# Kernel optimization log

Hardware: AMD Instinct MI355X
Metric: run time of the kernel (lower is better)

## Reference

```python
import jax, jax.numpy as jnp
import numpy as np

B, S, C = 256, 169, 512      # batch, input seq_len (hardcoded 169 in source), n_attn
H, TT, HS = 256, 256, 16     # n_head, ctx_len, head_size (all forced by hardcoded shapes)
OUT = 64                     # output Linear(16, 64)


def setup_inputs() -> dict:
    key = jax.random.key(0)
    ks = jax.random.split(key, 13)
    s_in = 1.0 / np.sqrt(C)
    s_hs = 1.0 / np.sqrt(HS)
    return {
        "x": jax.random.normal(ks[0], (B, S, C), dtype=jnp.float32),
        "time_w": jax.random.normal(ks[1], (H, TT), dtype=jnp.float32) * 0.1,
        "time_alpha": jax.random.normal(ks[2], (H, 1, TT), dtype=jnp.float32) * 0.1 + 1.0,
        "time_beta": jax.random.normal(ks[3], (H, TT, 1), dtype=jnp.float32) * 0.1 + 1.0,
        "time_gamma": jax.random.normal(ks[4], (TT, 1), dtype=jnp.float32) * 0.1 + 1.0,
        "key_w": jax.random.normal(ks[5], (HS, C), dtype=jnp.float32) * s_in,
        "key_b": jax.random.normal(ks[6], (HS,), dtype=jnp.float32) * s_in,
        "value_w": jax.random.normal(ks[7], (HS, C), dtype=jnp.float32) * s_in,
        "value_b": jax.random.normal(ks[8], (HS,), dtype=jnp.float32) * s_in,
        "recep_w": jax.random.normal(ks[9], (HS, C), dtype=jnp.float32) * s_in,
        "recep_b": jax.random.normal(ks[10], (HS,), dtype=jnp.float32) * s_in,
        "out_w": jax.random.normal(ks[11], (OUT, HS), dtype=jnp.float32) * s_hs,
        "out_b": jax.random.normal(ks[12], (OUT,), dtype=jnp.float32) * s_hs,
    }


def reference(x, time_w, time_alpha, time_beta, time_gamma,
              key_w, key_b, value_w, value_b, recep_w, recep_b,
              out_w, out_b):
    # --- build the time-decay matrix via the pad/tile shift trick ---
    w = jnp.pad(time_w, ((0, 0), (0, TT)))            # (H, 2TT)
    w = jnp.tile(w, (1, TT))                          # (H, 2TT*TT)
    w = w[:, :-TT].reshape(H, TT, 2 * TT - 1)
    w = w[:, :, TT - 1:]                              # (H, TT, TT)
    w = w * time_alpha * time_beta                    # (H, TT, TT)

    # --- channel-half time shift: first C/2 channels shifted back by 1 step ---
    half = C // 2
    shifted = jnp.pad(x[:, :, :half], ((0, 0), (1, 0), (0, 0)))[:, :-1]
    x = jnp.concatenate([shifted, x[:, :, half:]], axis=-1)

    # --- projections (torch Linear: y = x @ W.T + b) ---
    k = x @ key_w.T + key_b                           # (B, S, HS)
    v = x @ value_w.T + value_b
    r = x @ recep_w.T + recep_b

    pad_len = TT - S                                  # 256 - 169 = 87
    r = jnp.pad(r, ((0, 0), (0, pad_len), (0, 0)))    # (B, TT, HS)

    k = jnp.exp(jnp.clip(k, -60.0, 30.0))
    sum_k = jnp.cumsum(k, axis=1)                     # (B, S, HS)
    sum_k = jnp.pad(sum_k, ((0, 0), (0, pad_len), (0, 0)))  # (B, TT, HS)

    kv = k * v                                        # (B, S, HS)
    kv = jnp.pad(kv, ((0, 0), (0, pad_len), (0, 0)))  # (B, TT, HS)

    # einsum('htu,bhc->btc') == contract u first, then (t,h) matmul against kv's seq axis
    w2 = w.sum(axis=-1)                               # (H, TT): sum_u w[h,t,u]
    wkv = jnp.einsum('ht,bhc->btc', w2, kv)           # (B, TT, HS)

    # original divides by zero-padded sum_k in the padded tail; guard with 1 there
    denom = jnp.where(sum_k == 0, jnp.ones_like(sum_k), sum_k)
    rwkv = jax.nn.sigmoid(r) * wkv / denom            # (B, TT, HS)

    rwkv = rwkv @ out_w.T + out_b                     # (B, TT, 64)
    rwkv = rwkv * time_gamma[:TT]                     # (TT,1) broadcast
    return rwkv
```

## Files before the change

kernel.cpp:

```cpp
#include <hip/hip_runtime.h>

typedef unsigned short u16;
typedef unsigned int u32;
typedef __attribute__((ext_vector_type(8))) __bf16 bf16x8;
typedef __attribute__((ext_vector_type(4))) float f32x4;

#define S_LEN 169
#define C_DIM 512
#define SP 192

#define WT_OFF  0
#define XT0_OFF 49152
#define XT1_OFF 71680
#define KE_OFF  0
#define KVF_OFF 11264
#define RF_OFF  22528
#define KVT_OFF 33792
#define G_OFF   39936
#define RB_OFF  51200
#define SS_OFF  71680
#define OW_OFF  72704
#define LDS_BYTES 94208

#define LGKM_BAR() asm volatile("s_waitcnt lgkmcnt(0)\n\ts_barrier" ::: "memory")

__global__ __launch_bounds__(1024) void w2_kernel(
    const float* __restrict__ time_w,
    const float* __restrict__ time_alpha,
    const float* __restrict__ time_beta,
    __bf16* __restrict__ w2t)
{
    __shared__ float tw[256];
    __shared__ float al[256];
    __shared__ float part[4][256];
    const int s = blockIdx.x;
    const int t = threadIdx.x & 255;
    const int p = threadIdx.x >> 8;
    if (s >= S_LEN) {
        if (p == 0) w2t[t * SP + s] = (__bf16)0.f;
        return;
    }
    if (p == 0) { tw[t] = time_w[s * 256 + t]; al[t] = time_alpha[s * 256 + t]; }
    __syncthreads();
    const int u0 = p << 6;
    const int u1 = (u0 + 64 < t + 1) ? (u0 + 64) : (t + 1);
    float acc = 0.f;
    for (int u = u0; u < u1; ++u)
        acc = fmaf(tw[255 + u - t], al[u], acc);
    part[p][t] = acc;
    __syncthreads();
    if (p == 0)
        w2t[t * SP + s] = (__bf16)(time_beta[s * 256 + t] *
                                   (part[0][t] + part[1][t] + part[2][t] + part[3][t]));
}

__global__ __launch_bounds__(512) void rwkv_main(
    const float* __restrict__ x,
    const float* __restrict__ key_w, const float* __restrict__ key_b,
    const float* __restrict__ value_w, const float* __restrict__ value_b,
    const float* __restrict__ recep_w, const float* __restrict__ recep_b,
    const float* __restrict__ out_w, const float* __restrict__ out_b,
    const float* __restrict__ gamma,
    const __bf16* __restrict__ w2t,
    float* __restrict__ out)
{
    __shared__ __align__(16) char smem[LDS_BYTES];
    const int tid  = threadIdx.x;
    const int lane = tid & 63;
    const int wid  = tid >> 6;
    const int q    = lane >> 4;
    const int hs   = lane & 15;
    const int b    = blockIdx.x;
    const float* xb = x + (size_t)b * (S_LEN * C_DIM);

    for (int i = tid; i < 3072; i += 512) {
        int j  = i >> 6;
        int co = (i & 63) << 3;
        const float* src;
        if (j < 16)      src = key_w   + j * 512 + co;
        else if (j < 32) src = value_w + (j - 16) * 512 + co;
        else             src = recep_w + (j - 32) * 512 + co;
        float4 f0 = *(const float4*)src;
        float4 f1 = *(const float4*)(src + 4);
        bf16x8 p;
        p[0]=(__bf16)f0.x; p[1]=(__bf16)f0.y; p[2]=(__bf16)f0.z; p[3]=(__bf16)f0.w;
        p[4]=(__bf16)f1.x; p[5]=(__bf16)f1.y; p[6]=(__bf16)f1.z; p[7]=(__bf16)f1.w;
        u32 off = (((u32)j << 10) + ((u32)co << 1)) ^ (((u32)(j & 7)) << 4);
        *(bf16x8*)(smem + WT_OFF + off) = p;
    }

    const float kb = key_b[hs];
    const float vb = value_b[hs];
    const float rb = recep_b[hs];

    f32x4 acc0[3], acc1[3];
    #pragma unroll
    for (int n = 0; n < 3; ++n) { acc0[n] = (f32x4){0.f,0.f,0.f,0.f}; acc1[n] = (f32x4){0.f,0.f,0.f,0.f}; }
    const bool has_m1 = (wid < 3);

    float4 pfA[3][2]; int pvA[3];
    float4 pfB[3][2]; int pvB[3];

    auto ldchunk = [&](int chunk, float4 (&pf)[3][2], int (&pv)[3]) {
        const bool shifted = chunk < 4;
        #pragma unroll
        for (int it = 0; it < 3; ++it) {
            int i = tid + (it << 9);
            pv[it] = 0;
            if (i < 1408) {
                int r = i >> 3;
                int tsrc = shifted ? (r - 1) : r;
                bool valid = shifted ? (r >= 1 && r <= S_LEN) : (r < S_LEN);
                pv[it] = 1;
                if (valid) {
                    const float* src = xb + (size_t)tsrc * C_DIM + (chunk << 6) + ((i & 7) << 3);
                    pf[it][0] = *(const float4*)src;
                    pf[it][1] = *(const float4*)(src + 4);
                    pv[it] = 2;
                }
            }
        }
    };

    auto cvtwrite = [&](u32 base, float4 (&pf)[3][2], int (&pv)[3]) {
        #pragma unroll
        for (int it = 0; it < 3; ++it) {
            int i = tid + (it << 9);
            if (i < 1408 && pv[it]) {
                int r = i >> 3, co = (i & 7) << 3;
                bf16x8 p = {(__bf16)0.f,(__bf16)0.f,(__bf16)0.f,(__bf16)0.f,
                            (__bf16)0.f,(__bf16)0.f,(__bf16)0.f,(__bf16)0.f};
                if (pv[it] == 2) {
                    p[0]=(__bf16)pf[it][0].x; p[1]=(__bf16)pf[it][0].y;
                    p[2]=(__bf16)pf[it][0].z; p[3]=(__bf16)pf[it][0].w;
                    p[4]=(__bf16)pf[it][1].x; p[5]=(__bf16)pf[it][1].y;
                    p[6]=(__bf16)pf[it][1].z; p[7]=(__bf16)pf[it][1].w;
                }
                u32 off = (((u32)r << 7) + ((u32)co << 1)) ^ (((u32)(r & 7)) << 4);
                *(bf16x8*)(smem + base + off) = p;
            }
        }
    };

    auto mfma_chunk = [&](int chunk, u32 xbase) {
        #pragma unroll
        for (int ks = 0; ks < 2; ++ks) {
            int kc = ks << 5;
            bf16x8 bfr[3];
            #pragma unroll
            for (int nt = 0; nt < 3; ++nt) {
                int j = nt * 16 + hs;
                u32 col = (u32)((chunk << 6) + kc + (q << 3));
                u32 off = (((u32)j << 10) + (col << 1)) ^ (((u32)(j & 7)) << 4);
                bfr[nt] = *(const bf16x8*)(smem + WT_OFF + off);
            }
            {
                int row = wid * 16 + hs;
                u32 off = (((u32)row << 7) + ((u32)(kc + (q << 3)) << 1)) ^ (((u32)(row & 7)) << 4);
                bf16x8 afr = *(const bf16x8*)(smem + xbase + off);
                acc0[0] = __builtin_amdgcn_mfma_f32_16x16x32_bf16(afr, bfr[0], acc0[0], 0,0,0);
                acc0[1] = __builtin_amdgcn_mfma_f32_16x16x32_bf16(afr, bfr[1], acc0[1], 0,0,0);
                acc0[2] = __builtin_amdgcn_mfma_f32_16x16x32_bf16(afr, bfr[2], acc0[2], 0,0,0);
            }
            if (has_m1) {
                int row = (wid + 8) * 16 + hs;
                u32 off = (((u32)row << 7) + ((u32)(kc + (q << 3)) << 1)) ^ (((u32)(row & 7)) << 4);
                bf16x8 afr = *(const bf16x8*)(smem + xbase + off);
                acc1[0] = __builtin_amdgcn_mfma_f32_16x16x32_bf16(afr, bfr[0], acc1[0], 0,0,0);
                acc1[1] = __builtin_amdgcn_mfma_f32_16x16x32_bf16(afr, bfr[1], acc1[1], 0,0,0);
                acc1[2] = __builtin_amdgcn_mfma_f32_16x16x32_bf16(afr, bfr[2], acc1[2], 0,0,0);
            }
        }
    };

    ldchunk(0, pfA, pvA);
    cvtwrite(XT0_OFF, pfA, pvA);
    ldchunk(1, pfA, pvA);
    ldchunk(2, pfB, pvB);
    LGKM_BAR();

    #pragma unroll
    for (int chunk = 0; chunk < 8; ++chunk) {
        const u32 cur = (chunk & 1) ? XT1_OFF : XT0_OFF;
        const u32 nxt = (chunk & 1) ? XT0_OFF : XT1_OFF;
        mfma_chunk(chunk, cur);
        if (chunk < 7) {
            if (chunk & 1) cvtwrite(nxt, pfB, pvB);
            else           cvtwrite(nxt, pfA, pvA);
        }
        LGKM_BAR();
        if (chunk < 5) {
            if (chunk & 1) ldchunk(chunk + 3, pfB, pvB);
            else           ldchunk(chunk + 3, pfA, pvA);
        }
    }

    float* kef = (float*)(smem + KE_OFF);
    float* kvf = (float*)(smem + KVF_OFF);
    float* rff = (float*)(smem + RF_OFF);
    #pragma unroll
    for (int m = 0; m < 2; ++m) {
        if (m == 1 && !has_m1) break;
        const f32x4* A = (m == 0) ? acc0 : acc1;
        int tb = (wid + m * 8) * 16 + (q << 2);
        float ke[4];
        #pragma unroll
        for (int rg = 0; rg < 4; ++rg) {
            float kk = A[0][rg] + kb;
            kk = fminf(fmaxf(kk, -60.f), 30.f);
            ke[rg] = __expf(kk);
        }
        #pragma unroll
        for (int rg = 0; rg < 4; ++rg) {
            int t = tb + rg;
            kef[t * 16 + hs] = ke[rg];
            kvf[t * 16 + hs] = ke[rg] * (A[1][rg] + vb);
            rff[t * 16 + hs] = A[2][rg] + rb;
        }
    }
    __syncthreads();

    float* seg = (float*)(smem + SS_OFF);
    float* g   = (float*)(smem + G_OFF);
    if (tid < 256) {
        int h = tid & 15, sg = tid >> 4;
        int t0 = sg * 11, t1 = (t0 + 11 < S_LEN) ? t0 + 11 : S_LEN;
        float s = 0.f;
        for (int t = t0; t < t1; ++t) s += kef[t * 16 + h];
        seg[sg * 16 + h] = s;
    } else {
        int i2 = tid - 256;
        for (int i = i2; i < 4096; i += 256) {
            int row = i >> 4, c = 16 + (i & 15);
            ((__bf16*)(smem + RB_OFF))[row * 40 + c] = (__bf16)0.f;
        }
        for (int i = i2; i < 368; i += 256) {
            int h2 = i & 15; int t = S_LEN + (i >> 4);
            u32 off = ((u32)(h2 * 384 + t * 2)) ^ (((u32)(h2 & 7)) << 4);
            *(__bf16*)(smem + KVT_OFF + off) = (__bf16)0.f;
        }
        for (int i = i2; i < 2560; i += 256) {
            int o = i / 40, c = i - o * 40;
            ((__bf16*)(smem + OW_OFF))[o * 40 + c] = (c < 16) ? (__bf16)out_w[o * 16 + c] : (__bf16)0.f;
        }
    }
    __syncthreads();

    if (tid < 256) {
        int h = tid & 15, sg = tid >> 4;
        float run = 0.f;
        for (int s2 = 0; s2 < sg; ++s2) run += seg[s2 * 16 + h];
        int t0 = sg * 11, t1 = (t0 + 11 < S_LEN) ? t0 + 11 : S_LEN;
        for (int t = t0; t < t1; ++t) {
            run += kef[t * 16 + h];
            u32 off = ((u32)(h * 384 + t * 2)) ^ (((u32)(h & 7)) << 4);
            *(__bf16*)(smem + KVT_OFF + off) = (__bf16)kvf[t * 16 + h];
            float rr = rff[t * 16 + h];
            g[t * 16 + h] = 1.f / ((1.f + __expf(-rr)) * run);
        }
    }
    __syncthreads();

    f32x4 wa0 = (f32x4){0.f,0.f,0.f,0.f};
    f32x4 wa1 = (f32x4){0.f,0.f,0.f,0.f};
    #pragma unroll
    for (int s0 = 0; s0 < SP; s0 += 32) {
        int scol = s0 + (q << 3);
        u32 boff = ((u32)(hs * 384 + scol * 2)) ^ (((u32)(hs & 7)) << 4);
        bf16x8 bfr = *(const bf16x8*)(smem + KVT_OFF + boff);
        {
            int row = wid * 16 + hs;
            bf16x8 afr = *(const bf16x8*)(w2t + row * SP + scol);
            wa0 = __builtin_amdgcn_mfma_f32_16x16x32_bf16(afr, bfr, wa0, 0,0,0);
        }
        {
            int row = (wid + 8) * 16 + hs;
            bf16x8 afr = *(const bf16x8*)(w2t + row * SP + scol);
            wa1 = __builtin_amdgcn_mfma_f32_16x16x32_bf16(afr, bfr, wa1, 0,0,0);
        }
    }
    #pragma unroll
    for (int m = 0; m < 2; ++m) {
        const f32x4& W = (m == 0) ? wa0 : wa1;
        int tb = (wid + m * 8) * 16 + (q << 2);
        #pragma unroll
        for (int rg = 0; rg < 4; ++rg) {
            int t = tb + rg;
            float fac = (t < S_LEN) ? g[t * 16 + hs] : 0.5f;
            ((__bf16*)(smem + RB_OFF))[t * 40 + hs] = (__bf16)(W[rg] * fac);
        }
    }
    __syncthreads();

    float obv[4];
    #pragma unroll
    for (int nt = 0; nt < 4; ++nt) obv[nt] = out_b[nt * 16 + hs];
    #pragma unroll
    for (int m = 0; m < 2; ++m) {
        int mt = wid + m * 8;
        int arow = mt * 16 + hs;
        bf16x8 afr = *(const bf16x8*)(smem + RB_OFF + (u32)(arow * 80 + (q << 4)));
        float gm[4];
        #pragma unroll
        for (int rg = 0; rg < 4; ++rg) gm[rg] = gamma[mt * 16 + (q << 2) + rg];
        #pragma unroll
        for (int nt = 0; nt < 4; ++nt) {
            int orow = nt * 16 + hs;
            bf16x8 bfr = *(const bf16x8*)(smem + OW_OFF + (u32)(orow * 80 + (q << 4)));
            f32x4 zc = (f32x4){0.f,0.f,0.f,0.f};
            f32x4 d = __builtin_amdgcn_mfma_f32_16x16x32_bf16(afr, bfr, zc, 0,0,0);
            #pragma unroll
            for (int rg = 0; rg < 4; ++rg) {
                int t = mt * 16 + (q << 2) + rg;
                out[(size_t)b * 16384 + (size_t)t * 64 + nt * 16 + hs] = (d[rg] + obv[nt]) * gm[rg];
            }
        }
    }
}

extern "C" void kernel_launch(void* const* d_in, const int* in_sizes, int n_in,
                              void* d_out, int out_size, void* d_ws, size_t ws_size,
                              hipStream_t stream) {
    const float* x          = (const float*)d_in[0];
    const float* time_w     = (const float*)d_in[1];
    const float* time_alpha = (const float*)d_in[2];
    const float* time_beta  = (const float*)d_in[3];
    const float* time_gamma = (const float*)d_in[4];
    const float* key_w      = (const float*)d_in[5];
    const float* key_b      = (const float*)d_in[6];
    const float* value_w    = (const float*)d_in[7];
    const float* value_b    = (const float*)d_in[8];
    const float* recep_w    = (const float*)d_in[9];
    const float* recep_b    = (const float*)d_in[10];
    const float* out_w      = (const float*)d_in[11];
    const float* out_b      = (const float*)d_in[12];
    __bf16* w2t = (__bf16*)d_ws;

    w2_kernel<<<192, 1024, 0, stream>>>(time_w, time_alpha, time_beta, w2t);
    rwkv_main<<<256, 512, 0, stream>>>(x, key_w, key_b, value_w, value_b,
                                       recep_w, recep_b, out_w, out_b,
                                       time_gamma, w2t, (float*)d_out);
}
```

Before: 38.06 us.

## Split fused RWKV kernel into projection GEMM and scan kernels with workspace handoff

The single per-batch kernel is split into a GEMM kernel that handles half a sequence per block (512 blocks of 256 threads) and a separate scan/output kernel. The QKV weight bf16 packing moves into extra blocks of the w2 precompute kernel, so GEMM blocks copy pre-packed weights instead of converting them. The sigmoid is computed in the GEMM epilogue. The aim is more parallelism and less per-block LDS for the projection stage, at the cost of a global round-trip for k, kv and sigmoid(r) and an extra kernel launch.

```diff
diff --git a/kernel.cpp b/kernel.cpp
--- a/kernel.cpp
+++ b/kernel.cpp
@@ -6,21 +6,27 @@
 typedef __attribute__((ext_vector_type(4))) float f32x4;
 
 #define S_LEN 169
-#define C_DIM 512
 #define SP 192
+
+#define W2T_WS 0
+#define WPK_WS 98304
+#define KE_WS  147456
+#define KV_WS  3031040
+#define SG_WS  5914624
 
 #define WT_OFF  0
 #define XT0_OFF 49152
-#define XT1_OFF 71680
-#define KE_OFF  0
-#define KVF_OFF 11264
-#define RF_OFF  22528
-#define KVT_OFF 33792
-#define G_OFF   39936
-#define RB_OFF  51200
-#define SS_OFF  71680
-#define OW_OFF  72704
-#define LDS_BYTES 94208
+#define XT1_OFF 61440
+#define G_LDS   73728
+
+#define SKE  0
+#define SKV  11264
+#define SG2  22528
+#define SKVT 33792
+#define SRB  39936
+#define SSS  60416
+#define SOW  61440
+#define S_LDS 66560
 
 #define LGKM_BAR() asm volatile("s_waitcnt lgkmcnt(0)\n\ts_barrier" ::: "memory")
 
@@ -28,12 +34,37 @@
     const float* __restrict__ time_w,
     const float* __restrict__ time_alpha,
     const float* __restrict__ time_beta,
-    __bf16* __restrict__ w2t)
+    const float* __restrict__ key_w,
+    const float* __restrict__ value_w,
+    const float* __restrict__ recep_w,
+    char* __restrict__ ws)
 {
+    __bf16* w2t = (__bf16*)(ws + W2T_WS);
+    const int blk = blockIdx.x;
+    if (blk >= 192) {
+        int p = blk - 192;
+        int u = threadIdx.x;
+        if (u < 768) {
+            int j  = 12 * p + (u >> 6);
+            int co = (u & 63) << 3;
+            const float* src;
+            if (j < 16)      src = key_w   + j * 512 + co;
+            else if (j < 32) src = value_w + (j - 16) * 512 + co;
+            else             src = recep_w + (j - 32) * 512 + co;
+            float4 f0 = *(const float4*)src;
+            float4 f1 = *(const float4*)(src + 4);
+            bf16x8 pk;
+            pk[0]=(__bf16)f0.x; pk[1]=(__bf16)f0.y; pk[2]=(__bf16)f0.z; pk[3]=(__bf16)f0.w;
+            pk[4]=(__bf16)f1.x; pk[5]=(__bf16)f1.y; pk[6]=(__bf16)f1.z; pk[7]=(__bf16)f1.w;
+            u32 off = (((u32)j << 10) + ((u32)co << 1)) ^ (((u32)(j & 7)) << 4);
+            *(bf16x8*)(ws + WPK_WS + off) = pk;
+        }
+        return;
+    }
     __shared__ float tw[256];
     __shared__ float al[256];
     __shared__ float part[4][256];
-    const int s = blockIdx.x;
+    const int s = blk;
     const int t = threadIdx.x & 255;
     const int p = threadIdx.x >> 8;
     if (s >= S_LEN) {
@@ -54,39 +85,31 @@
                                    (part[0][t] + part[1][t] + part[2][t] + part[3][t]));
 }
 
-__global__ __launch_bounds__(512) void rwkv_main(
+__global__ __launch_bounds__(256) void gemm_kernel(
     const float* __restrict__ x,
-    const float* __restrict__ key_w, const float* __restrict__ key_b,
-    const float* __restrict__ value_w, const float* __restrict__ value_b,
-    const float* __restrict__ recep_w, const float* __restrict__ recep_b,
-    const float* __restrict__ out_w, const float* __restrict__ out_b,
-    const float* __restrict__ gamma,
-    const __bf16* __restrict__ w2t,
-    float* __restrict__ out)
+    const float* __restrict__ key_b,
+    const float* __restrict__ value_b,
+    const float* __restrict__ recep_b,
+    const char* __restrict__ wsr,
+    char* __restrict__ ws)
 {
-    __shared__ __align__(16) char smem[LDS_BYTES];
+    __shared__ __align__(16) char smem[G_LDS];
     const int tid  = threadIdx.x;
     const int lane = tid & 63;
     const int wid  = tid >> 6;
     const int q    = lane >> 4;
     const int hs   = lane & 15;
-    const int b    = blockIdx.x;
-    const float* xb = x + (size_t)b * (S_LEN * C_DIM);
-
-    for (int i = tid; i < 3072; i += 512) {
-        int j  = i >> 6;
-        int co = (i & 63) << 3;
-        const float* src;
-        if (j < 16)      src = key_w   + j * 512 + co;
-        else if (j < 32) src = value_w + (j - 16) * 512 + co;
-        else             src = recep_w + (j - 32) * 512 + co;
-        float4 f0 = *(const float4*)src;
-        float4 f1 = *(const float4*)(src + 4);
-        bf16x8 p;
-        p[0]=(__bf16)f0.x; p[1]=(__bf16)f0.y; p[2]=(__bf16)f0.z; p[3]=(__bf16)f0.w;
-        p[4]=(__bf16)f1.x; p[5]=(__bf16)f1.y; p[6]=(__bf16)f1.z; p[7]=(__bf16)f1.w;
-        u32 off = (((u32)j << 10) + ((u32)co << 1)) ^ (((u32)(j & 7)) << 4);
-        *(bf16x8*)(smem + WT_OFF + off) = p;
+    const int b    = blockIdx.x >> 1;
+    const int half = blockIdx.x & 1;
+    const int t0   = half * 88;
+    const int nrows = half ? 81 : 88;
+    const float* xb = x + (size_t)b * (S_LEN * 512);
+
+    #pragma unroll
+    for (int it = 0; it < 12; ++it) {
+        int i = tid + (it << 8);
+        uint4 cp = *(const uint4*)(wsr + WPK_WS + i * 16);
+        *(uint4*)(smem + WT_OFF + i * 16) = cp;
     }
 
     const float kb = key_b[hs];
@@ -96,7 +119,7 @@
     f32x4 acc0[3], acc1[3];
     #pragma unroll
     for (int n = 0; n < 3; ++n) { acc0[n] = (f32x4){0.f,0.f,0.f,0.f}; acc1[n] = (f32x4){0.f,0.f,0.f,0.f}; }
-    const bool has_m1 = (wid < 3);
+    const bool has_m1 = (wid < 2);
 
     float4 pfA[3][2]; int pvA[3];
     float4 pfB[3][2]; int pvB[3];
@@ -105,19 +128,15 @@
         const bool shifted = chunk < 4;
         #pragma unroll
         for (int it = 0; it < 3; ++it) {
-            int i = tid + (it << 9);
-            pv[it] = 0;
-            if (i < 1408) {
-                int r = i >> 3;
-                int tsrc = shifted ? (r - 1) : r;
-                bool valid = shifted ? (r >= 1 && r <= S_LEN) : (r < S_LEN);
-                pv[it] = 1;
-                if (valid) {
-                    const float* src = xb + (size_t)tsrc * C_DIM + (chunk << 6) + ((i & 7) << 3);
-                    pf[it][0] = *(const float4*)src;
-                    pf[it][1] = *(const float4*)(src + 4);
-                    pv[it] = 2;
-                }
+            int i = tid + (it << 8);
+            int r = i >> 3;
+            bool valid = shifted ? (r < nrows && (t0 + r) >= 1) : (r < nrows);
+            pv[it] = valid ? 1 : 0;
+            if (valid) {
+                int tsrc = t0 + r - (shifted ? 1 : 0);
+                const float* src = xb + (size_t)tsrc * 512 + (chunk << 6) + ((i & 7) << 3);
+                pf[it][0] = *(const float4*)src;
+                pf[it][1] = *(const float4*)(src + 4);
             }
         }
     };
@@ -125,20 +144,18 @@
     auto cvtwrite = [&](u32 base, float4 (&pf)[3][2], int (&pv)[3]) {
         #pragma unroll
         for (int it = 0; it < 3; ++it) {
-            int i = tid + (it << 9);
-            if (i < 1408 && pv[it]) {
-                int r = i >> 3, co = (i & 7) << 3;
-                bf16x8 p = {(__bf16)0.f,(__bf16)0.f,(__bf16)0.f,(__bf16)0.f,
-                            (__bf16)0.f,(__bf16)0.f,(__bf16)0.f,(__bf16)0.f};
-                if (pv[it] == 2) {
-                    p[0]=(__bf16)pf[it][0].x; p[1]=(__bf16)pf[it][0].y;
-                    p[2]=(__bf16)pf[it][0].z; p[3]=(__bf16)pf[it][0].w;
-                    p[4]=(__bf16)pf[it][1].x; p[5]=(__bf16)pf[it][1].y;
-                    p[6]=(__bf16)pf[it][1].z; p[7]=(__bf16)pf[it][1].w;
-                }
-                u32 off = (((u32)r << 7) + ((u32)co << 1)) ^ (((u32)(r & 7)) << 4);
-                *(bf16x8*)(smem + base + off) = p;
-            }
+            int i = tid + (it << 8);
+            int r = i >> 3, co = (i & 7) << 3;
+            bf16x8 p = {(__bf16)0.f,(__bf16)0.f,(__bf16)0.f,(__bf16)0.f,
+                        (__bf16)0.f,(__bf16)0.f,(__bf16)0.f,(__bf16)0.f};
+            if (pv[it]) {
+                p[0]=(__bf16)pf[it][0].x; p[1]=(__bf16)pf[it][0].y;
+                p[2]=(__bf16)pf[it][0].z; p[3]=(__bf16)pf[it][0].w;
+                p[4]=(__bf16)pf[it][1].x; p[5]=(__bf16)pf[it][1].y;
+                p[6]=(__bf16)pf[it][1].z; p[7]=(__bf16)pf[it][1].w;
+            }
+            u32 off = (((u32)r << 7) + ((u32)co << 1)) ^ (((u32)(r & 7)) << 4);
+            *(bf16x8*)(smem + base + off) = p;
         }
     };
 
@@ -163,7 +180,7 @@
                 acc0[2] = __builtin_amdgcn_mfma_f32_16x16x32_bf16(afr, bfr[2], acc0[2], 0,0,0);
             }
             if (has_m1) {
-                int row = (wid + 8) * 16 + hs;
+                int row = (wid + 4) * 16 + hs;
                 u32 off = (((u32)row << 7) + ((u32)(kc + (q << 3)) << 1)) ^ (((u32)(row & 7)) << 4);
                 bf16x8 afr = *(const bf16x8*)(smem + xbase + off);
                 acc1[0] = __builtin_amdgcn_mfma_f32_16x16x32_bf16(afr, bfr[0], acc1[0], 0,0,0);
@@ -195,99 +212,121 @@
         }
     }
 
-    float* kef = (float*)(smem + KE_OFF);
-    float* kvf = (float*)(smem + KVF_OFF);
-    float* rff = (float*)(smem + RF_OFF);
+    float* keg = (float*)(ws + KE_WS);
+    float* kvg = (float*)(ws + KV_WS);
+    float* sgg = (float*)(ws + SG_WS);
     #pragma unroll
     for (int m = 0; m < 2; ++m) {
         if (m == 1 && !has_m1) break;
         const f32x4* A = (m == 0) ? acc0 : acc1;
-        int tb = (wid + m * 8) * 16 + (q << 2);
-        float ke[4];
+        int tl = (wid + m * 4) * 16 + (q << 2);
         #pragma unroll
         for (int rg = 0; rg < 4; ++rg) {
-            float kk = A[0][rg] + kb;
-            kk = fminf(fmaxf(kk, -60.f), 30.f);
-            ke[rg] = __expf(kk);
-        }
-        #pragma unroll
-        for (int rg = 0; rg < 4; ++rg) {
-            int t = tb + rg;
-            kef[t * 16 + hs] = ke[rg];
-            kvf[t * 16 + hs] = ke[rg] * (A[1][rg] + vb);
-            rff[t * 16 + hs] = A[2][rg] + rb;
-        }
-    }
-    __syncthreads();
-
-    float* seg = (float*)(smem + SS_OFF);
-    float* g   = (float*)(smem + G_OFF);
-    if (tid < 256) {
-        int h = tid & 15, sg = tid >> 4;
-        int t0 = sg * 11, t1 = (t0 + 11 < S_LEN) ? t0 + 11 : S_LEN;
-        float s = 0.f;
-        for (int t = t0; t < t1; ++t) s += kef[t * 16 + h];
-        seg[sg * 16 + h] = s;
-    } else {
-        int i2 = tid - 256;
-        for (int i = i2; i < 4096; i += 256) {
-            int row = i >> 4, c = 16 + (i & 15);
-            ((__bf16*)(smem + RB_OFF))[row * 40 + c] = (__bf16)0.f;
-        }
-        for (int i = i2; i < 368; i += 256) {
-            int h2 = i & 15; int t = S_LEN + (i >> 4);
-            u32 off = ((u32)(h2 * 384 + t * 2)) ^ (((u32)(h2 & 7)) << 4);
-            *(__bf16*)(smem + KVT_OFF + off) = (__bf16)0.f;
-        }
-        for (int i = i2; i < 2560; i += 256) {
-            int o = i / 40, c = i - o * 40;
-            ((__bf16*)(smem + OW_OFF))[o * 40 + c] = (c < 16) ? (__bf16)out_w[o * 16 + c] : (__bf16)0.f;
-        }
-    }
-    __syncthreads();
-
-    if (tid < 256) {
-        int h = tid & 15, sg = tid >> 4;
+            int t_local = tl + rg;
+            if (t_local < nrows) {
+                int t = t0 + t_local;
+                float kk = fminf(fmaxf(A[0][rg] + kb, -60.f), 30.f);
+                float ke = __expf(kk);
+                size_t o = ((size_t)b * 176 + t) * 16 + hs;
+                keg[o] = ke;
+                kvg[o] = ke * (A[1][rg] + vb);
+                sgg[o] = 1.f / (1.f + __expf(-(A[2][rg] + rb)));
+            }
+        }
+    }
+}
+
+__global__ __launch_bounds__(256) void scan_kernel(
+    const char* __restrict__ wsr,
+    const float* __restrict__ out_w, const float* __restrict__ out_b,
+    const float* __restrict__ gamma,
+    float* __restrict__ out)
+{
+    __shared__ __align__(16) char smem[S_LDS];
+    const int tid  = threadIdx.x;
+    const int lane = tid & 63;
+    const int wid  = tid >> 6;
+    const int q    = lane >> 4;
+    const int hs   = lane & 15;
+    const int b    = blockIdx.x;
+    const __bf16* w2t = (const __bf16*)(wsr + W2T_WS);
+    const float4* keb = (const float4*)(wsr + KE_WS + (size_t)b * 11264);
+    const float4* kvb = (const float4*)(wsr + KV_WS + (size_t)b * 11264);
+    const float4* sgb = (const float4*)(wsr + SG_WS + (size_t)b * 11264);
+
+    #pragma unroll
+    for (int it = 0; it < 3; ++it) {
+        int i = tid + (it << 8);
+        if (i < 676) {
+            ((float4*)(smem + SKE))[i] = keb[i];
+            ((float4*)(smem + SKV))[i] = kvb[i];
+            ((float4*)(smem + SG2))[i] = sgb[i];
+        }
+    }
+    for (int i = tid; i < 2560; i += 256) {
+        int o = i / 40, c = i - o * 40;
+        ((__bf16*)(smem + SOW))[i] = (c < 16) ? (__bf16)out_w[o * 16 + c] : (__bf16)0.f;
+    }
+    for (int i = tid; i < 4096; i += 256) {
+        int row = i >> 4, c = 16 + (i & 15);
+        ((__bf16*)(smem + SRB))[row * 40 + c] = (__bf16)0.f;
+    }
+    for (int i = tid; i < 368; i += 256) {
+        int h2 = i & 15; int t = S_LEN + (i >> 4);
+        u32 off = ((u32)(h2 * 384 + t * 2)) ^ (((u32)(h2 & 7)) << 4);
+        *(__bf16*)(smem + SKVT + off) = (__bf16)0.f;
+    }
+    __syncthreads();
+
+    float* KE = (float*)(smem + SKE);
+    float* KV = (float*)(smem + SKV);
+    float* GG = (float*)(smem + SG2);
+    float* SEG = (float*)(smem + SSS);
+    const int h  = tid & 15;
+    const int sg = tid >> 4;
+    const int ts = sg * 11;
+    const int te = (ts + 11 < S_LEN) ? ts + 11 : S_LEN;
+    {
+        float ssum = 0.f;
+        for (int t = ts; t < te; ++t) ssum += KE[t * 16 + h];
+        SEG[sg * 16 + h] = ssum;
+    }
+    __syncthreads();
+    {
         float run = 0.f;
-        for (int s2 = 0; s2 < sg; ++s2) run += seg[s2 * 16 + h];
-        int t0 = sg * 11, t1 = (t0 + 11 < S_LEN) ? t0 + 11 : S_LEN;
-        for (int t = t0; t < t1; ++t) {
-            run += kef[t * 16 + h];
+        for (int s2 = 0; s2 < sg; ++s2) run += SEG[s2 * 16 + h];
+        for (int t = ts; t < te; ++t) {
+            run += KE[t * 16 + h];
             u32 off = ((u32)(h * 384 + t * 2)) ^ (((u32)(h & 7)) << 4);
-            *(__bf16*)(smem + KVT_OFF + off) = (__bf16)kvf[t * 16 + h];
-            float rr = rff[t * 16 + h];
-            g[t * 16 + h] = 1.f / ((1.f + __expf(-rr)) * run);
-        }
-    }
-    __syncthreads();
-
-    f32x4 wa0 = (f32x4){0.f,0.f,0.f,0.f};
-    f32x4 wa1 = (f32x4){0.f,0.f,0.f,0.f};
+            *(__bf16*)(smem + SKVT + off) = (__bf16)KV[t * 16 + h];
+            GG[t * 16 + h] = GG[t * 16 + h] / run;
+        }
+    }
+    __syncthreads();
+
+    f32x4 wa[4];
+    #pragma unroll
+    for (int mi = 0; mi < 4; ++mi) wa[mi] = (f32x4){0.f,0.f,0.f,0.f};
     #pragma unroll
     for (int s0 = 0; s0 < SP; s0 += 32) {
         int scol = s0 + (q << 3);
         u32 boff = ((u32)(hs * 384 + scol * 2)) ^ (((u32)(hs & 7)) << 4);
-        bf16x8 bfr = *(const bf16x8*)(smem + KVT_OFF + boff);
-        {
-            int row = wid * 16 + hs;
+        bf16x8 bfr = *(const bf16x8*)(smem + SKVT + boff);
+        #pragma unroll
+        for (int mi = 0; mi < 4; ++mi) {
+            int row = (wid + (mi << 2)) * 16 + hs;
             bf16x8 afr = *(const bf16x8*)(w2t + row * SP + scol);
-            wa0 = __builtin_amdgcn_mfma_f32_16x16x32_bf16(afr, bfr, wa0, 0,0,0);
-        }
-        {
-            int row = (wid + 8) * 16 + hs;
-            bf16x8 afr = *(const bf16x8*)(w2t + row * SP + scol);
-            wa1 = __builtin_amdgcn_mfma_f32_16x16x32_bf16(afr, bfr, wa1, 0,0,0);
-        }
-    }
-    #pragma unroll
-    for (int m = 0; m < 2; ++m) {
-        const f32x4& W = (m == 0) ? wa0 : wa1;
-        int tb = (wid + m * 8) * 16 + (q << 2);
+            wa[mi] = __builtin_amdgcn_mfma_f32_16x16x32_bf16(afr, bfr, wa[mi], 0,0,0);
+        }
+    }
+    #pragma unroll
+    for (int mi = 0; mi < 4; ++mi) {
+        int tb = (wid + (mi << 2)) * 16 + (q << 2);
         #pragma unroll
         for (int rg = 0; rg < 4; ++rg) {
             int t = tb + rg;
-            float fac = (t < S_LEN) ? g[t * 16 + hs] : 0.5f;
-            ((__bf16*)(smem + RB_OFF))[t * 40 + hs] = (__bf16)(W[rg] * fac);
+            float fac = (t < S_LEN) ? GG[t * 16 + hs] : 0.5f;
+            ((__bf16*)(smem + SRB))[t * 40 + hs] = (__bf16)(wa[mi][rg] * fac);
         }
     }
     __syncthreads();
@@ -296,17 +335,17 @@
     #pragma unroll
     for (int nt = 0; nt < 4; ++nt) obv[nt] = out_b[nt * 16 + hs];
     #pragma unroll
-    for (int m = 0; m < 2; ++m) {
-        int mt = wid + m * 8;
+    for (int mi = 0; mi < 4; ++mi) {
+        int mt = wid + (mi << 2);
         int arow = mt * 16 + hs;
-        bf16x8 afr = *(const bf16x8*)(smem + RB_OFF + (u32)(arow * 80 + (q << 4)));
+        bf16x8 afr = *(const bf16x8*)(smem + SRB + (u32)(arow * 80 + (q << 4)));
         float gm[4];
         #pragma unroll
         for (int rg = 0; rg < 4; ++rg) gm[rg] = gamma[mt * 16 + (q << 2) + rg];
         #pragma unroll
         for (int nt = 0; nt < 4; ++nt) {
             int orow = nt * 16 + hs;
-            bf16x8 bfr = *(const bf16x8*)(smem + OW_OFF + (u32)(orow * 80 + (q << 4)));
+            bf16x8 bfr = *(const bf16x8*)(smem + SOW + (u32)(orow * 80 + (q << 4)));
             f32x4 zc = (f32x4){0.f,0.f,0.f,0.f};
             f32x4 d = __builtin_amdgcn_mfma_f32_16x16x32_bf16(afr, bfr, zc, 0,0,0);
             #pragma unroll
@@ -334,10 +373,10 @@
     const float* recep_b    = (const float*)d_in[10];
     const float* out_w      = (const float*)d_in[11];
     const float* out_b      = (const float*)d_in[12];
-    __bf16* w2t = (__bf16*)d_ws;
-
-    w2_kernel<<<192, 1024, 0, stream>>>(time_w, time_alpha, time_beta, w2t);
-    rwkv_main<<<256, 512, 0, stream>>>(x, key_w, key_b, value_w, value_b,
-                                       recep_w, recep_b, out_w, out_b,
-                                       time_gamma, w2t, (float*)d_out);
+    char* ws = (char*)d_ws;
+
+    w2_kernel<<<196, 1024, 0, stream>>>(time_w, time_alpha, time_beta,
+                                        key_w, value_w, recep_w, ws);
+    gemm_kernel<<<512, 256, 0, stream>>>(x, key_b, value_b, recep_b, ws, ws);
+    scan_kernel<<<256, 256, 0, stream>>>(ws, out_w, out_b, time_gamma, (float*)d_out);
 }
```

New measurement: 41.61 us. 1.09x slower.
